# Optimization experiments

Measured on AMD Instinct MI355X. Metric: run time of the kernel, lower is better.

The kernel has to match this reference:

```python
import jax, jax.numpy as jnp
import numpy as np
from jax import lax

B, T, C, DIN, DOUT = 32, 128, 64, 32, 32  # batch, output_channels(seq), input_channels, input_dim, output_dim


def _init_params(key):
    # Mirror torch init: xOps zeros with identity on min(dout,din) diag; hOps = eye.
    # Add small noise so gradients/behavior are non-degenerate.
    k1, k2 = jax.random.split(key)
    eye_x = jnp.zeros((DOUT, DIN), jnp.float32).at[jnp.arange(min(DOUT, DIN)), jnp.arange(min(DOUT, DIN))].set(1.0)
    xOps = jnp.broadcast_to(eye_x, (4, T, C, DOUT, DIN)) + 0.02 * jax.random.normal(k1, (4, T, C, DOUT, DIN), jnp.float32)
    hOps = jnp.broadcast_to(jnp.eye(DOUT, dtype=jnp.float32), (4, T, C, DOUT, DOUT)) + 0.02 * jax.random.normal(k2, (4, T, C, DOUT, DOUT), jnp.float32)
    return xOps, hOps


def setup_inputs() -> dict:
    key = jax.random.key(0)
    kx, kp = jax.random.split(key)
    x = jax.random.normal(kx, (B, T, C, DIN), jnp.float32)
    xOps, hOps = _init_params(kp)
    return {"x": x, "xOps": xOps, "hOps": hOps}


def reference(x, xOps, hOps):
    # x: [B,T,C,Din]; xOps: [4,T,C,Dout,Din]; hOps: [4,T,C,Dout,Dout]
    b, t, c, _ = x.shape
    dout = hOps.shape[-1]
    h0 = jnp.zeros((b, c, dout), x.dtype)
    c0 = jnp.zeros((b, c, dout), x.dtype)

    def step(carry, inp):
        h, cc = carry
        x_t, xop_t, hop_t = inp  # [B,C,Din], [4,C,Dout,Din], [4,C,Dout,Dout]
        # per-channel (grouped) gate pre-activations, 4 gates at once
        X = jnp.einsum('gcij,bcj->gbci', xop_t, x_t) + jnp.einsum('gcij,bcj->gbci', hop_t, h)
        i = jax.nn.sigmoid(X[0])
        f = jax.nn.sigmoid(X[1])
        g = jnp.tanh(X[2])
        o = jax.nn.sigmoid(X[3])
        c_new = f * cc + i * g
        h_new = o * jnp.tanh(c_new)
        return (h_new, c_new), None

    xs = (jnp.swapaxes(x, 0, 1), jnp.swapaxes(xOps, 0, 1), jnp.swapaxes(hOps, 0, 1))
    (h_fin, _), _ = lax.scan(step, (h0, c0), xs)
    return h_fin  # [B,C,Dout]
```

## Files before the change

kernel.cpp:

```cpp
#include <hip/hip_runtime.h>
#include <stdint.h>

#define T_STEPS 128
#define C_CH    64

using frag_ab = __attribute__((ext_vector_type(8))) short;
using frag_cd = __attribute__((ext_vector_type(4))) float;
typedef __attribute__((ext_vector_type(4))) uint32_t u32x4;

__device__ __forceinline__ uint32_t pack_hi16(uint32_t u0, uint32_t u1) {
  return __builtin_amdgcn_perm(u1, u0, 0x07060302u);
}

__device__ __forceinline__ float fast_sigmoid(float v) {
  return __builtin_amdgcn_rcpf(1.0f + __expf(-v));
}
__device__ __forceinline__ float fast_tanh(float v) {
  return fmaf(2.0f, __builtin_amdgcn_rcpf(1.0f + __expf(-2.0f * v)), -1.0f);
}

__device__ __forceinline__ void async_load16(const float* g, void* l) {
  __builtin_amdgcn_global_load_lds((const __attribute__((address_space(1))) void*)g,
                                   (__attribute__((address_space(3))) void*)l, 16, 0, 0);
}

struct Frag2 { frag_ab hi, lo; };

__device__ __forceinline__ Frag2 split8(float4 a, float4 b) {
  uint32_t u0 = __float_as_uint(a.x), u1 = __float_as_uint(a.y);
  uint32_t u2 = __float_as_uint(a.z), u3 = __float_as_uint(a.w);
  uint32_t u4 = __float_as_uint(b.x), u5 = __float_as_uint(b.y);
  uint32_t u6 = __float_as_uint(b.z), u7 = __float_as_uint(b.w);
  uint32_t r0 = __float_as_uint(a.x - __uint_as_float(u0 & 0xFFFF0000u));
  uint32_t r1 = __float_as_uint(a.y - __uint_as_float(u1 & 0xFFFF0000u));
  uint32_t r2 = __float_as_uint(a.z - __uint_as_float(u2 & 0xFFFF0000u));
  uint32_t r3 = __float_as_uint(a.w - __uint_as_float(u3 & 0xFFFF0000u));
  uint32_t r4 = __float_as_uint(b.x - __uint_as_float(u4 & 0xFFFF0000u));
  uint32_t r5 = __float_as_uint(b.y - __uint_as_float(u5 & 0xFFFF0000u));
  uint32_t r6 = __float_as_uint(b.z - __uint_as_float(u6 & 0xFFFF0000u));
  uint32_t r7 = __float_as_uint(b.w - __uint_as_float(u7 & 0xFFFF0000u));
  union { u32x4 v; frag_ab f; } H, L;
  H.v[0] = pack_hi16(u0, u1); H.v[1] = pack_hi16(u2, u3);
  H.v[2] = pack_hi16(u4, u5); H.v[3] = pack_hi16(u6, u7);
  L.v[0] = pack_hi16(r0, r1); L.v[1] = pack_hi16(r2, r3);
  L.v[2] = pack_hi16(r4, r5); L.v[3] = pack_hi16(r6, r7);
  Frag2 o; o.hi = H.f; o.lo = L.f; return o;
}

__global__ void __launch_bounds__(512)
lstm_kernel(const float* __restrict__ x, const float* __restrict__ xOps,
            const float* __restrict__ hOps, float* __restrict__ out) {
  __shared__ __align__(16) float Afp[2][2][128][32];
  __shared__ __align__(16) short Bq[2][2][2][4][16][8];

  const int tid    = threadIdx.x;
  const int c      = blockIdx.x & 63;
  const int q      = blockIdx.x >> 6;
  const int w      = tid >> 6;
  const int lane   = tid & 63;
  const int frag_n = lane & 15;
  const int quad   = lane >> 4;

  int apl[4], arb[4];
  const float* aptr[4];
#pragma unroll
  for (int ii = 0; ii < 4; ++ii) {
    const int idx = w + 8 * ii;
    const int pl  = idx >> 4;
    const int rb  = idx & 15;
    apl[ii] = pl; arb[ii] = rb;
    const int r    = rb * 8 + (lane >> 3);
    const int g    = r >> 5;
    const int i    = r & 31;
    const int f    = ((r >> 5) << 1) | (r & 1);
    const int slot = (lane & 7) ^ f;
    const float* base = pl ? hOps : xOps;
    aptr[ii] = base + ((size_t)g * T_STEPS * C_CH + c) * 1024
                    + (size_t)i * 32 + slot * 4;
  }

  const bool xthr = (tid < 128);
  const int  xn   = (tid >> 4) & 7;
  const int  xjp  = (tid & 15) * 2;
  const float* xptr = x + (size_t)(q * 8 + xn) * (T_STEPS * C_CH * 32)
                        + c * 32 + xjp;

  for (int idx = tid; idx < 4096; idx += 512) ((uint32_t*)Bq)[idx] = 0u;
  __syncthreads();

#pragma unroll
  for (int ii = 0; ii < 4; ++ii) {
    async_load16(aptr[ii], &Afp[0][apl[ii]][arb[ii] * 8][0]);
    aptr[ii] += (size_t)C_CH * 1024;
  }
  float2 xv = make_float2(0.f, 0.f);
  if (xthr) {
    float2 x0 = *(const float2*)xptr;
    uint32_t u0 = __float_as_uint(x0.x), u1 = __float_as_uint(x0.y);
    float r0 = x0.x - __uint_as_float(u0 & 0xFFFF0000u);
    float r1 = x0.y - __uint_as_float(u1 & 0xFFFF0000u);
    const int kg = xjp >> 3, sl = xjp & 7;
    *(uint32_t*)&Bq[0][0][0][kg][xn][sl] = pack_hi16(u0, u1);
    *(uint32_t*)&Bq[0][0][1][kg][xn][sl] =
        pack_hi16(__float_as_uint(r0), __float_as_uint(r1));
    xv = *(const float2*)(xptr + (size_t)C_CH * 32);
  }
  asm volatile("s_waitcnt vmcnt(0) lgkmcnt(0)\n\ts_barrier" ::: "memory");

  const int frow = (frag_n & 3) * 32 + 4 * w + (frag_n >> 2);
  const int ff   = ((frow >> 5) << 1) | (frow & 1);
  const int so0  = (((quad << 1) ^ ff) << 2);
  const int so1  = ((((quad << 1) | 1) ^ ff) << 2);
  const int iq   = 4 * w + quad;
  const int hkg  = iq >> 3, hsl = iq & 7;

  float c_state = 0.0f;

#pragma unroll 2
  for (int t = 0; t < T_STEPS; ++t) {
    const int cb = t & 1, nb = cb ^ 1;

    if (t + 1 < T_STEPS) {
#pragma unroll
      for (int ii = 0; ii < 4; ++ii) {
        async_load16(aptr[ii], &Afp[nb][apl[ii]][arb[ii] * 8][0]);
        aptr[ii] += (size_t)C_CH * 1024;
      }
      if (xthr) {
        uint32_t u0 = __float_as_uint(xv.x), u1 = __float_as_uint(xv.y);
        float r0 = xv.x - __uint_as_float(u0 & 0xFFFF0000u);
        float r1 = xv.y - __uint_as_float(u1 & 0xFFFF0000u);
        const int kg = xjp >> 3, sl = xjp & 7;
        *(uint32_t*)&Bq[nb][0][0][kg][xn][sl] = pack_hi16(u0, u1);
        *(uint32_t*)&Bq[nb][0][1][kg][xn][sl] =
            pack_hi16(__float_as_uint(r0), __float_as_uint(r1));
        if (t + 2 < T_STEPS)
          xv = *(const float2*)(xptr + (size_t)(t + 2) * (C_CH * 32));
      }
    }

    frag_cd acc = {0.f, 0.f, 0.f, 0.f};
#pragma unroll
    for (int kt = 0; kt < 2; ++kt) {
      const float* Ap = &Afp[cb][kt][frow][0];
      const float4 va = *(const float4*)(Ap + so0);
      const float4 vb = *(const float4*)(Ap + so1);
      Frag2 A = split8(va, vb);
      const frag_ab bh = *(const frag_ab*)&Bq[cb][kt][0][quad][frag_n][0];
      const frag_ab bl = *(const frag_ab*)&Bq[cb][kt][1][quad][frag_n][0];
      acc = __builtin_amdgcn_mfma_f32_16x16x32_bf16(A.hi, bh, acc, 0, 0, 0);
      acc = __builtin_amdgcn_mfma_f32_16x16x32_bf16(A.hi, bl, acc, 0, 0, 0);
      acc = __builtin_amdgcn_mfma_f32_16x16x32_bf16(A.lo, bh, acc, 0, 0, 0);
    }

    const float ig = fast_sigmoid(acc[0]);
    const float fg = fast_sigmoid(acc[1]);
    const float gg = fast_tanh(acc[2]);
    const float og = fast_sigmoid(acc[3]);
    c_state = fg * c_state + ig * gg;
    const float hval = og * fast_tanh(c_state);

    if (t == T_STEPS - 1) {
      if (frag_n < 8)
        out[((size_t)(q * 8 + frag_n) * C_CH + c) * 32 + iq] = hval;
    } else {
      uint32_t uh = __float_as_uint(hval);
      float    rh = hval - __uint_as_float(uh & 0xFFFF0000u);
      uint32_t ur = __float_as_uint(rh);
      uint32_t pu = __shfl_xor(uh, 16);
      uint32_t pr = __shfl_xor(ur, 16);
      if (((quad & 1) == 0) && (frag_n < 8)) {
        *(uint32_t*)&Bq[nb][1][0][hkg][frag_n][hsl] = pack_hi16(uh, pu);
        *(uint32_t*)&Bq[nb][1][1][hkg][frag_n][hsl] = pack_hi16(ur, pr);
      }
      asm volatile("s_waitcnt vmcnt(0) lgkmcnt(0)\n\ts_barrier" ::: "memory");
    }
  }
}

extern "C" void kernel_launch(void* const* d_in, const int* in_sizes, int n_in,
                              void* d_out, int out_size, void* d_ws, size_t ws_size,
                              hipStream_t stream) {
  const float* x    = (const float*)d_in[0];
  const float* xOps = (const float*)d_in[1];
  const float* hOps = (const float*)d_in[2];
  lstm_kernel<<<dim3(256), dim3(512), 0, stream>>>(x, xOps, hOps, (float*)d_out);
}
```

Measured before the change: 406.5 us.

## Deepen async prefetch to four stages and stage x/h as fp32 in LDS

```diff
diff --git a/kernel.cpp b/kernel.cpp
--- a/kernel.cpp
+++ b/kernel.cpp
@@ -3,6 +3,7 @@
 
 #define T_STEPS 128
 #define C_CH    64
+#define PIPE    4
 
 using frag_ab = __attribute__((ext_vector_type(8))) short;
 using frag_cd = __attribute__((ext_vector_type(4))) float;
@@ -50,8 +51,10 @@
 __global__ void __launch_bounds__(512)
 lstm_kernel(const float* __restrict__ x, const float* __restrict__ xOps,
             const float* __restrict__ hOps, float* __restrict__ out) {
-  __shared__ __align__(16) float Afp[2][2][128][32];
-  __shared__ __align__(16) short Bq[2][2][2][4][16][8];
+  __shared__ __align__(16) float Afp[PIPE][2][128][32];
+  __shared__ __align__(16) float Bx[PIPE][16][32];
+  __shared__ __align__(16) float Bh[2][16][32];
+  __shared__ __align__(16) float Scr[256];
 
   const int tid    = threadIdx.x;
   const int c      = blockIdx.x & 63;
@@ -79,78 +82,80 @@
                     + (size_t)i * 32 + slot * 4;
   }
 
-  const bool xthr = (tid < 128);
-  const int  xn   = (tid >> 4) & 7;
-  const int  xjp  = (tid & 15) * 2;
-  const float* xptr = x + (size_t)(q * 8 + xn) * (T_STEPS * C_CH * 32)
-                        + c * 32 + xjp;
+  const int xn  = lane >> 3, xsl = lane & 7;
+  const float* xsrc = x + (((size_t)(q * 8 + xn) * T_STEPS) * C_CH + c) * 32
+                        + ((xsl ^ (xn & 7)) << 2);
+  const float* dummy_src = xOps;
 
-  for (int idx = tid; idx < 4096; idx += 512) ((uint32_t*)Bq)[idx] = 0u;
+  for (int i = tid; i < 2 * 16 * 32; i += 512) ((float*)Bh)[i] = 0.f;
+  for (int i = tid; i < PIPE * 16 * 32; i += 512) ((float*)Bx)[i] = 0.f;
   __syncthreads();
 
 #pragma unroll
-  for (int ii = 0; ii < 4; ++ii) {
-    async_load16(aptr[ii], &Afp[0][apl[ii]][arb[ii] * 8][0]);
-    aptr[ii] += (size_t)C_CH * 1024;
+  for (int s0 = 0; s0 < PIPE - 1; ++s0) {
+#pragma unroll
+    for (int ii = 0; ii < 4; ++ii) {
+      async_load16(aptr[ii], &Afp[s0][apl[ii]][arb[ii] * 8][0]);
+      aptr[ii] += (size_t)C_CH * 1024;
+    }
+    if (w == 7) { async_load16(xsrc, &Bx[s0][0][0]); xsrc += (size_t)C_CH * 32; }
   }
-  float2 xv = make_float2(0.f, 0.f);
-  if (xthr) {
-    float2 x0 = *(const float2*)xptr;
-    uint32_t u0 = __float_as_uint(x0.x), u1 = __float_as_uint(x0.y);
-    float r0 = x0.x - __uint_as_float(u0 & 0xFFFF0000u);
-    float r1 = x0.y - __uint_as_float(u1 & 0xFFFF0000u);
-    const int kg = xjp >> 3, sl = xjp & 7;
-    *(uint32_t*)&Bq[0][0][0][kg][xn][sl] = pack_hi16(u0, u1);
-    *(uint32_t*)&Bq[0][0][1][kg][xn][sl] =
-        pack_hi16(__float_as_uint(r0), __float_as_uint(r1));
-    xv = *(const float2*)(xptr + (size_t)C_CH * 32);
-  }
-  asm volatile("s_waitcnt vmcnt(0) lgkmcnt(0)\n\ts_barrier" ::: "memory");
 
   const int frow = (frag_n & 3) * 32 + 4 * w + (frag_n >> 2);
   const int ff   = ((frow >> 5) << 1) | (frow & 1);
   const int so0  = (((quad << 1) ^ ff) << 2);
   const int so1  = ((((quad << 1) | 1) ^ ff) << 2);
+  const int bs0  = (((quad << 1) ^ (frag_n & 7)) << 2);
+  const int bs1  = ((((quad << 1) | 1) ^ (frag_n & 7)) << 2);
   const int iq   = 4 * w + quad;
-  const int hkg  = iq >> 3, hsl = iq & 7;
+  const int hwi  = ((w ^ (frag_n & 7)) << 2) | quad;
 
   float c_state = 0.0f;
 
-#pragma unroll 2
+#pragma unroll 4
   for (int t = 0; t < T_STEPS; ++t) {
-    const int cb = t & 1, nb = cb ^ 1;
+    const int cb = t & (PIPE - 1);
+    const int hp = t & 1;
 
-    if (t + 1 < T_STEPS) {
+    if (w == 7) asm volatile("s_waitcnt vmcnt(10) lgkmcnt(0)" ::: "memory");
+    else        asm volatile("s_waitcnt vmcnt(8) lgkmcnt(0)" ::: "memory");
+    asm volatile("s_barrier" ::: "memory");
+
+    {
+      const int s = t + PIPE - 1;
+      if (s < T_STEPS) {
+        const int sb = s & (PIPE - 1);
 #pragma unroll
-      for (int ii = 0; ii < 4; ++ii) {
-        async_load16(aptr[ii], &Afp[nb][apl[ii]][arb[ii] * 8][0]);
-        aptr[ii] += (size_t)C_CH * 1024;
-      }
-      if (xthr) {
-        uint32_t u0 = __float_as_uint(xv.x), u1 = __float_as_uint(xv.y);
-        float r0 = xv.x - __uint_as_float(u0 & 0xFFFF0000u);
-        float r1 = xv.y - __uint_as_float(u1 & 0xFFFF0000u);
-        const int kg = xjp >> 3, sl = xjp & 7;
-        *(uint32_t*)&Bq[nb][0][0][kg][xn][sl] = pack_hi16(u0, u1);
-        *(uint32_t*)&Bq[nb][0][1][kg][xn][sl] =
-            pack_hi16(__float_as_uint(r0), __float_as_uint(r1));
-        if (t + 2 < T_STEPS)
-          xv = *(const float2*)(xptr + (size_t)(t + 2) * (C_CH * 32));
+        for (int ii = 0; ii < 4; ++ii) {
+          async_load16(aptr[ii], &Afp[sb][apl[ii]][arb[ii] * 8][0]);
+          aptr[ii] += (size_t)C_CH * 1024;
+        }
+        if (w == 7) { async_load16(xsrc, &Bx[sb][0][0]); xsrc += (size_t)C_CH * 32; }
+      } else {
+#pragma unroll
+        for (int ii = 0; ii < 4; ++ii) async_load16(dummy_src, &Scr[0]);
+        if (w == 7) async_load16(dummy_src, &Scr[0]);
       }
     }
 
     frag_cd acc = {0.f, 0.f, 0.f, 0.f};
-#pragma unroll
-    for (int kt = 0; kt < 2; ++kt) {
-      const float* Ap = &Afp[cb][kt][frow][0];
-      const float4 va = *(const float4*)(Ap + so0);
-      const float4 vb = *(const float4*)(Ap + so1);
-      Frag2 A = split8(va, vb);
-      const frag_ab bh = *(const frag_ab*)&Bq[cb][kt][0][quad][frag_n][0];
-      const frag_ab bl = *(const frag_ab*)&Bq[cb][kt][1][quad][frag_n][0];
-      acc = __builtin_amdgcn_mfma_f32_16x16x32_bf16(A.hi, bh, acc, 0, 0, 0);
-      acc = __builtin_amdgcn_mfma_f32_16x16x32_bf16(A.hi, bl, acc, 0, 0, 0);
-      acc = __builtin_amdgcn_mfma_f32_16x16x32_bf16(A.lo, bh, acc, 0, 0, 0);
+    {
+      const float* Ap = &Afp[cb][0][frow][0];
+      Frag2 A = split8(*(const float4*)(Ap + so0), *(const float4*)(Ap + so1));
+      const float* Bp = &Bx[cb][frag_n][0];
+      Frag2 Bf = split8(*(const float4*)(Bp + bs0), *(const float4*)(Bp + bs1));
+      acc = __builtin_amdgcn_mfma_f32_16x16x32_bf16(A.hi, Bf.hi, acc, 0, 0, 0);
+      acc = __builtin_amdgcn_mfma_f32_16x16x32_bf16(A.hi, Bf.lo, acc, 0, 0, 0);
+      acc = __builtin_amdgcn_mfma_f32_16x16x32_bf16(A.lo, Bf.hi, acc, 0, 0, 0);
+    }
+    {
+      const float* Ap = &Afp[cb][1][frow][0];
+      Frag2 A = split8(*(const float4*)(Ap + so0), *(const float4*)(Ap + so1));
+      const float* Bp = &Bh[hp][frag_n][0];
+      Frag2 Bf = split8(*(const float4*)(Bp + bs0), *(const float4*)(Bp + bs1));
+      acc = __builtin_amdgcn_mfma_f32_16x16x32_bf16(A.hi, Bf.hi, acc, 0, 0, 0);
+      acc = __builtin_amdgcn_mfma_f32_16x16x32_bf16(A.hi, Bf.lo, acc, 0, 0, 0);
+      acc = __builtin_amdgcn_mfma_f32_16x16x32_bf16(A.lo, Bf.hi, acc, 0, 0, 0);
     }
 
     const float ig = fast_sigmoid(acc[0]);
@@ -164,16 +169,7 @@
       if (frag_n < 8)
         out[((size_t)(q * 8 + frag_n) * C_CH + c) * 32 + iq] = hval;
     } else {
-      uint32_t uh = __float_as_uint(hval);
-      float    rh = hval - __uint_as_float(uh & 0xFFFF0000u);
-      uint32_t ur = __float_as_uint(rh);
-      uint32_t pu = __shfl_xor(uh, 16);
-      uint32_t pr = __shfl_xor(ur, 16);
-      if (((quad & 1) == 0) && (frag_n < 8)) {
-        *(uint32_t*)&Bq[nb][1][0][hkg][frag_n][hsl] = pack_hi16(uh, pu);
-        *(uint32_t*)&Bq[nb][1][1][hkg][frag_n][hsl] = pack_hi16(ur, pr);
-      }
-      asm volatile("s_waitcnt vmcnt(0) lgkmcnt(0)\n\ts_barrier" ::: "memory");
+      if (frag_n < 8) Bh[hp ^ 1][frag_n][hwi] = hval;
     }
   }
 }
```

Result: faster. 335.4 us (-17.5%).
